# Kernel tuning notes

Measured on AMD Instinct MI355X. Metric: run time of the kernel, lower is better.

Reference implementation:

```python
import jax, jax.numpy as jnp
import numpy as np

K = 1024
D = 256
COMMITMENT_WEIGHT = 0.25


def setup_inputs() -> dict:
    key = jax.random.key(0)
    kz, kw = jax.random.split(key)
    z = jax.random.normal(kz, (16, 4096, D), dtype=jnp.float32)
    # nn.init.uniform_(weight, -1/K, 1/K)
    emb = jax.random.uniform(kw, (K, D), dtype=jnp.float32, minval=-1.0 / K, maxval=1.0 / K)
    return {"z": z, "emb": emb}


def reference(z, emb):
    B, N, _ = z.shape
    flat = z.reshape(-1, D)                                  # [BN, D]
    dist = (jnp.sum(flat * flat, axis=1, keepdims=True)
            - 2.0 * flat @ emb.T
            + jnp.sum(emb * emb, axis=1))                    # [BN, K]
    indices = jnp.argmin(dist, axis=1)                       # [BN]
    z_q = emb[indices].reshape(z.shape)                      # [B, N, D]
    codebook_loss = jnp.mean((z_q - jax.lax.stop_gradient(z)) ** 2)
    commitment_loss = jnp.mean((z - jax.lax.stop_gradient(z_q)) ** 2)
    loss = codebook_loss + COMMITMENT_WEIGHT * commitment_loss
    z_q_st = z + jax.lax.stop_gradient(z_q - z)              # straight-through
    return z_q_st, loss, indices.reshape(B, N)
```

## Files before the change

### kernel.cpp

```cpp
#include <hip/hip_runtime.h>


constexpr int D      = 256;
constexpr int KC     = 1024;
constexpr int BM     = 64;
constexpr int BN     = 64;
constexpr int NROWS  = 16 * 4096;
constexpr long long ZQ_N = (long long)NROWS * D;

__device__ __forceinline__ float np_half_sumsq(const float* a, int s) {
    float r[8];
#pragma unroll
    for (int j = 0; j < 8; ++j) r[j] = __fmul_rn(a[j * s], a[j * s]);
    for (int i = 8; i < 128; i += 8)
#pragma unroll
        for (int j = 0; j < 8; ++j)
            r[j] = __fadd_rn(r[j], __fmul_rn(a[(i + j) * s], a[(i + j) * s]));
    return __fadd_rn(__fadd_rn(__fadd_rn(r[0], r[1]), __fadd_rn(r[2], r[3])),
                     __fadd_rn(__fadd_rn(r[4], r[5]), __fadd_rn(r[6], r[7])));
}
__device__ __forceinline__ float np_sumsq_256(const float* a, int s) {
    return __fadd_rn(np_half_sumsq(a, s), np_half_sumsq(a + 128 * s, s));
}

__global__ __launch_bounds__(256) void vq_prep(const float* __restrict__ emb,
                                               float* __restrict__ se32,
                                               double* __restrict__ acc) {
    int k = blockIdx.x * 256 + threadIdx.x;
    if (k < KC) se32[k] = np_sumsq_256(emb + (size_t)k * D, 1);
    if (k == 0) *acc = 0.0;
}

__global__ __launch_bounds__(256) void vq_main(const float* __restrict__ z,
                                               const float* __restrict__ emb,
                                               const float* __restrict__ se32,
                                               float* __restrict__ out_zq,
                                               float* __restrict__ out_idx1,
                                               float* __restrict__ out_idx2,
                                               double* __restrict__ acc) {
    __shared__ float xs[D][BM];
    __shared__ float es[32][BN];
    __shared__ float sxs[BM];
    __shared__ int   code_of_row[BM];
    __shared__ float wave_part[4];

    const int tid = threadIdx.x;
    const int tx  = tid & 15;
    const int ty  = tid >> 4;
    const int r0  = blockIdx.x * BM;

    {
        int r = tid >> 2;
        int dbase = (tid & 3) << 6;
        const float* zp = z + (size_t)(r0 + r) * D + dbase;
#pragma unroll
        for (int j = 0; j < 16; ++j) {
            float4 v = *(const float4*)(zp + 4 * j);
            int d = dbase + 4 * j;
            xs[d + 0][r] = v.x; xs[d + 1][r] = v.y;
            xs[d + 2][r] = v.z; xs[d + 3][r] = v.w;
        }
    }
    __syncthreads();
    if (tid < BM) sxs[tid] = np_sumsq_256(&xs[0][tid], BM);

    float bestv[4];
    int   bestk[4];
#pragma unroll
    for (int i = 0; i < 4; ++i) { bestv[i] = 3.0e38f; bestk[i] = 0; }

    for (int kt = 0; kt < KC / BN; ++kt) {
        const int k0 = kt * BN;
        double a[4][4];
#pragma unroll
        for (int i = 0; i < 4; ++i)
#pragma unroll
            for (int j = 0; j < 4; ++j) a[i][j] = 0.0;

        for (int dc = 0; dc < D / 32; ++dc) {
            const int d0 = dc * 32;
            __syncthreads();
            {
                int c  = tid >> 2;
                int dd = (tid & 3) << 3;
                const float* ep = emb + (size_t)(k0 + c) * D + d0 + dd;
                float4 v0 = *(const float4*)(ep);
                float4 v1 = *(const float4*)(ep + 4);
                es[dd + 0][c] = v0.x; es[dd + 1][c] = v0.y;
                es[dd + 2][c] = v0.z; es[dd + 3][c] = v0.w;
                es[dd + 4][c] = v1.x; es[dd + 5][c] = v1.y;
                es[dd + 6][c] = v1.z; es[dd + 7][c] = v1.w;
            }
            __syncthreads();
#pragma unroll
            for (int kk = 0; kk < 32; ++kk) {
                float4 xv = *(const float4*)&xs[d0 + kk][ty << 2];
                float4 ev = *(const float4*)&es[kk][tx << 2];
                double xd[4] = { xv.x, xv.y, xv.z, xv.w };
                double ed[4] = { ev.x, ev.y, ev.z, ev.w };
#pragma unroll
                for (int i = 0; i < 4; ++i)
#pragma unroll
                    for (int j = 0; j < 4; ++j)
                        a[i][j] = __fma_rn(xd[i], ed[j], a[i][j]);
            }
        }
#pragma unroll
        for (int j = 0; j < 4; ++j) {
            int k = k0 + (tx << 2) + j;
            float se = se32[k];
#pragma unroll
            for (int i = 0; i < 4; ++i) {
                float sx  = sxs[(ty << 2) + i];
                float g32 = (float)a[i][j];
                float t   = __fadd_rn(__fsub_rn(sx, 2.0f * g32), se);
                if (t < bestv[i]) { bestv[i] = t; bestk[i] = k; }
            }
        }
    }

    __syncthreads();
    float* red_val = &es[0][0];
    int*   red_idx = (int*)&es[16][0];
#pragma unroll
    for (int i = 0; i < 4; ++i) {
        int r = (ty << 2) + i;
        red_val[r * 16 + tx] = bestv[i];
        red_idx[r * 16 + tx] = bestk[i];
    }
    __syncthreads();
    if (tid < BM) {
        int r = tid;
        float bv = 3.0e38f; int bk = 1 << 30;
#pragma unroll
        for (int t = 0; t < 16; ++t) {
            float v  = red_val[r * 16 + t];
            int   id = red_idx[r * 16 + t];
            if (v < bv || (v == bv && id < bk)) { bv = v; bk = id; }
        }
        code_of_row[r] = bk;
        out_idx1[r0 + r] = (float)bk;
        out_idx2[r0 + r] = (float)bk;
    }
    __syncthreads();

    float ls = 0.f;
    {
        int r = tid >> 2;
        int dbase = (tid & 3) << 6;
        int c = code_of_row[r];
        const float* ep = emb + (size_t)c * D + dbase;
        float* op = out_zq + (size_t)(r0 + r) * D + dbase;
#pragma unroll
        for (int j = 0; j < 16; ++j) {
            float4 e4 = *(const float4*)(ep + 4 * j);
            int d = dbase + 4 * j;
            float d0v = e4.x - xs[d + 0][r];
            float d1v = e4.y - xs[d + 1][r];
            float d2v = e4.z - xs[d + 2][r];
            float d3v = e4.w - xs[d + 3][r];
            ls += d0v * d0v + d1v * d1v + d2v * d2v + d3v * d3v;
            *(float4*)(op + 4 * j) = e4;
        }
    }
#pragma unroll
    for (int off = 32; off > 0; off >>= 1) ls += __shfl_down(ls, off);
    if ((tid & 63) == 0) wave_part[tid >> 6] = ls;
    __syncthreads();
    if (tid == 0) {
        double t = (double)wave_part[0] + (double)wave_part[1]
                 + (double)wave_part[2] + (double)wave_part[3];
        atomicAdd(acc, t);
    }
}

__global__ void vq_finalize(const double* __restrict__ acc,
                            float* __restrict__ l1, float* __restrict__ l2) {
    double m = *acc / (double)ZQ_N;
    float v = (float)(1.25 * m);
    *l1 = v; *l2 = v;
}

extern "C" void kernel_launch(void* const* d_in, const int* in_sizes, int n_in,
                              void* d_out, int out_size, void* d_ws, size_t ws_size,
                              hipStream_t stream) {
    const float* z   = (const float*)d_in[0];
    const float* emb = (const float*)d_in[1];
    float* out = (float*)d_out;

    float* out_zq    = out;
    float* out_loss1 = out + ZQ_N;
    float* out_idx1  = out + ZQ_N + 1;
    size_t osz = (size_t)out_size;
    float* out_idx2  = out + (osz - (size_t)NROWS);
    float* out_loss2 = out + (osz - (size_t)NROWS - 1);

    float*  se32 = (float*)d_ws;
    double* acc  = (double*)((char*)d_ws + 4096);

    vq_prep<<<4, 256, 0, stream>>>(emb, se32, acc);
    vq_main<<<NROWS / BM, 256, 0, stream>>>(z, emb, se32, out_zq, out_idx1,
                                            out_idx2, acc);
    vq_finalize<<<1, 1, 0, stream>>>(acc, out_loss1, out_loss2);
}
```

Baseline: 1.441 ms.

## Use FP32 distance GEMM and rescore near-tie rows in double precision

```diff
diff --git a/kernel.cpp b/kernel.cpp
--- a/kernel.cpp
+++ b/kernel.cpp
@@ -7,6 +7,8 @@
 constexpr int BN     = 64;
 constexpr int NROWS  = 16 * 4096;
 constexpr long long ZQ_N = (long long)NROWS * D;
+constexpr float MARGIN = 2e-4f;
+constexpr int  CAP   = 32768;
 
 __device__ __forceinline__ float np_half_sumsq(const float* a, int s) {
     float r[8];
@@ -25,10 +27,11 @@
 
 __global__ __launch_bounds__(256) void vq_prep(const float* __restrict__ emb,
                                                float* __restrict__ se32,
-                                               double* __restrict__ acc) {
+                                               double* __restrict__ acc,
+                                               int* __restrict__ cnt) {
     int k = blockIdx.x * 256 + threadIdx.x;
     if (k < KC) se32[k] = np_sumsq_256(emb + (size_t)k * D, 1);
-    if (k == 0) *acc = 0.0;
+    if (k == 0) { *acc = 0.0; *cnt = 0; }
 }
 
 __global__ __launch_bounds__(256) void vq_main(const float* __restrict__ z,
@@ -37,9 +40,12 @@
                                                float* __restrict__ out_zq,
                                                float* __restrict__ out_idx1,
                                                float* __restrict__ out_idx2,
-                                               double* __restrict__ acc) {
+                                               double* __restrict__ acc,
+                                               int* __restrict__ cnt,
+                                               int* __restrict__ rowlist) {
     __shared__ float xs[D][BM];
     __shared__ float es[32][BN];
+    __shared__ float red_sec[BM * 16];
     __shared__ float sxs[BM];
     __shared__ int   code_of_row[BM];
     __shared__ float wave_part[4];
@@ -64,18 +70,18 @@
     __syncthreads();
     if (tid < BM) sxs[tid] = np_sumsq_256(&xs[0][tid], BM);
 
-    float bestv[4];
+    float bestv[4], secv[4];
     int   bestk[4];
 #pragma unroll
-    for (int i = 0; i < 4; ++i) { bestv[i] = 3.0e38f; bestk[i] = 0; }
+    for (int i = 0; i < 4; ++i) { bestv[i] = 3.0e38f; secv[i] = 3.0e38f; bestk[i] = 0; }
 
     for (int kt = 0; kt < KC / BN; ++kt) {
         const int k0 = kt * BN;
-        double a[4][4];
+        float a[4][4];
 #pragma unroll
         for (int i = 0; i < 4; ++i)
 #pragma unroll
-            for (int j = 0; j < 4; ++j) a[i][j] = 0.0;
+            for (int j = 0; j < 4; ++j) a[i][j] = 0.f;
 
         for (int dc = 0; dc < D / 32; ++dc) {
             const int d0 = dc * 32;
@@ -96,13 +102,13 @@
             for (int kk = 0; kk < 32; ++kk) {
                 float4 xv = *(const float4*)&xs[d0 + kk][ty << 2];
                 float4 ev = *(const float4*)&es[kk][tx << 2];
-                double xd[4] = { xv.x, xv.y, xv.z, xv.w };
-                double ed[4] = { ev.x, ev.y, ev.z, ev.w };
+                float xr[4] = { xv.x, xv.y, xv.z, xv.w };
+                float er[4] = { ev.x, ev.y, ev.z, ev.w };
 #pragma unroll
                 for (int i = 0; i < 4; ++i)
 #pragma unroll
                     for (int j = 0; j < 4; ++j)
-                        a[i][j] = __fma_rn(xd[i], ed[j], a[i][j]);
+                        a[i][j] = fmaf(xr[i], er[j], a[i][j]);
             }
         }
 #pragma unroll
@@ -111,10 +117,9 @@
             float se = se32[k];
 #pragma unroll
             for (int i = 0; i < 4; ++i) {
-                float sx  = sxs[(ty << 2) + i];
-                float g32 = (float)a[i][j];
-                float t   = __fadd_rn(__fsub_rn(sx, 2.0f * g32), se);
-                if (t < bestv[i]) { bestv[i] = t; bestk[i] = k; }
+                float t = (sxs[(ty << 2) + i] - 2.0f * a[i][j]) + se;
+                if (t < bestv[i]) { secv[i] = bestv[i]; bestv[i] = t; bestk[i] = k; }
+                else if (t < secv[i]) { secv[i] = t; }
             }
         }
     }
@@ -127,20 +132,31 @@
         int r = (ty << 2) + i;
         red_val[r * 16 + tx] = bestv[i];
         red_idx[r * 16 + tx] = bestk[i];
+        red_sec[r * 16 + tx] = secv[i];
     }
     __syncthreads();
     if (tid < BM) {
         int r = tid;
-        float bv = 3.0e38f; int bk = 1 << 30;
+        float b1 = 3.0e38f; int k1 = 1 << 30; int t1 = 0;
 #pragma unroll
         for (int t = 0; t < 16; ++t) {
             float v  = red_val[r * 16 + t];
             int   id = red_idx[r * 16 + t];
-            if (v < bv || (v == bv && id < bk)) { bv = v; bk = id; }
-        }
-        code_of_row[r] = bk;
-        out_idx1[r0 + r] = (float)bk;
-        out_idx2[r0 + r] = (float)bk;
+            if (v < b1 || (v == b1 && id < k1)) { b1 = v; k1 = id; t1 = t; }
+        }
+        float b2 = 3.0e38f;
+#pragma unroll
+        for (int t = 0; t < 16; ++t) {
+            float v = (t == t1) ? red_sec[r * 16 + t] : red_val[r * 16 + t];
+            if (v < b2) b2 = v;
+        }
+        code_of_row[r] = k1;
+        out_idx1[r0 + r] = (float)k1;
+        out_idx2[r0 + r] = (float)k1;
+        if (b2 - b1 <= MARGIN) {
+            int slot = atomicAdd(cnt, 1);
+            if (slot < CAP) rowlist[slot] = r0 + r;
+        }
     }
     __syncthreads();
 
@@ -174,6 +190,50 @@
     }
 }
 
+__global__ __launch_bounds__(256) void vq_rescore(const float* __restrict__ z,
+                                                  const float* __restrict__ emb,
+                                                  const float* __restrict__ se32,
+                                                  float* __restrict__ out_idx1,
+                                                  float* __restrict__ out_idx2,
+                                                  const int* __restrict__ rowlist,
+                                                  const int* __restrict__ cnt) {
+    int gw   = (blockIdx.x * blockDim.x + threadIdx.x) >> 6;
+    int nw   = (gridDim.x * blockDim.x) >> 6;
+    int lane = threadIdx.x & 63;
+    int n = *cnt; if (n > CAP) n = CAP;
+    for (int li = gw; li < n; li += nw) {
+        int row = rowlist[li];
+        const float*  x  = z + (size_t)row * D;
+        const float4* xp = (const float4*)x;
+        float sx = np_sumsq_256(x, 1);
+        float bt = 3.0e38f; int bk = 1 << 30;
+        for (int c = 0; c < 16; ++c) {
+            int k = c * 64 + lane;
+            const float4* ep = (const float4*)(emb + (size_t)k * D);
+            double s = 0.0;
+#pragma unroll 8
+            for (int q = 0; q < 64; ++q) {
+                float4 ev = ep[q];
+                float4 xv = xp[q];
+                s = fma((double)xv.x, (double)ev.x, s);
+                s = fma((double)xv.y, (double)ev.y, s);
+                s = fma((double)xv.z, (double)ev.z, s);
+                s = fma((double)xv.w, (double)ev.w, s);
+            }
+            float g = (float)s;
+            float t = __fadd_rn(__fsub_rn(sx, 2.0f * g), se32[k]);
+            if (t < bt) { bt = t; bk = k; }
+        }
+#pragma unroll
+        for (int off = 32; off > 0; off >>= 1) {
+            float ot = __shfl_xor(bt, off);
+            int   ok = __shfl_xor(bk, off);
+            if (ot < bt || (ot == bt && ok < bk)) { bt = ot; bk = ok; }
+        }
+        if (lane == 0) { out_idx1[row] = (float)bk; out_idx2[row] = (float)bk; }
+    }
+}
+
 __global__ void vq_finalize(const double* __restrict__ acc,
                             float* __restrict__ l1, float* __restrict__ l2) {
     double m = *acc / (double)ZQ_N;
@@ -195,11 +255,15 @@
     float* out_idx2  = out + (osz - (size_t)NROWS);
     float* out_loss2 = out + (osz - (size_t)NROWS - 1);
 
-    float*  se32 = (float*)d_ws;
-    double* acc  = (double*)((char*)d_ws + 4096);
-
-    vq_prep<<<4, 256, 0, stream>>>(emb, se32, acc);
+    float*  se32    = (float*)d_ws;
+    double* acc     = (double*)((char*)d_ws + 4096);
+    int*    cnt     = (int*)((char*)d_ws + 4104);
+    int*    rowlist = (int*)((char*)d_ws + 8192);
+
+    vq_prep<<<4, 256, 0, stream>>>(emb, se32, acc, cnt);
     vq_main<<<NROWS / BM, 256, 0, stream>>>(z, emb, se32, out_zq, out_idx1,
-                                            out_idx2, acc);
+                                            out_idx2, acc, cnt, rowlist);
+    vq_rescore<<<256, 256, 0, stream>>>(z, emb, se32, out_idx1, out_idx2,
+                                        rowlist, cnt);
     vq_finalize<<<1, 1, 0, stream>>>(acc, out_loss1, out_loss2);
 }
```

Measured after the change: 1.510 ms. +4.8%, slower.
